# Kernel optimization log

Measured on AMD Instinct MI355X. Metric: run time of the kernel, lower is better.

## Reference

```python
import jax, jax.numpy as jnp
import numpy as np
from jax import lax

B, S, H, T = 64, 512, 1024, 21


def setup_inputs() -> dict:
    key = jax.random.key(0)
    k1, k2, k3, k4, k5, k6, k7 = jax.random.split(key, 7)
    hidden_states = jax.random.normal(k1, (B, S, H), dtype=jnp.float32)
    attention_mask = jnp.ones((B, S), dtype=jnp.int32)
    labels = jax.random.randint(k2, (B, S), 0, T).astype(jnp.int64)
    W = jax.random.normal(k3, (T, H), dtype=jnp.float32) * 0.02
    b = jnp.zeros((T,), dtype=jnp.float32)
    # torchcrf init: uniform(-0.1, 0.1)
    transitions = jax.random.uniform(k4, (T, T), minval=-0.1, maxval=0.1, dtype=jnp.float32)
    start_transitions = jax.random.uniform(k5, (T,), minval=-0.1, maxval=0.1, dtype=jnp.float32)
    end_transitions = jax.random.uniform(k6, (T,), minval=-0.1, maxval=0.1, dtype=jnp.float32)
    return {
        "hidden_states": hidden_states,
        "attention_mask": attention_mask,
        "labels": labels,
        "W": W,
        "b": b,
        "transitions": transitions,
        "start_transitions": start_transitions,
        "end_transitions": end_transitions,
    }


def _crf_log_likelihood(emissions, labels, mask, trans, start, end):
    # emissions [B,S,T], labels [B,S] int, mask [B,S] bool. reduction='sum'.
    Bn, Sn, Tn = emissions.shape
    maskf = mask.astype(emissions.dtype)
    emit_scores = jnp.take_along_axis(emissions, labels[:, :, None], axis=2)[:, :, 0]  # [B,S]
    trans_scores = trans[labels[:, :-1], labels[:, 1:]]  # [B,S-1]
    numerator = start[labels[:, 0]] + emit_scores[:, 0]
    numerator = numerator + jnp.sum((trans_scores + emit_scores[:, 1:]) * maskf[:, 1:], axis=1)
    seq_ends = jnp.sum(mask.astype(jnp.int32), axis=1) - 1  # [B]
    last_tags = labels[jnp.arange(Bn), seq_ends]
    numerator = numerator + end[last_tags]
    # partition via forward algorithm (scan over time)
    alpha0 = start[None, :] + emissions[:, 0]  # [B,T]
    def step(alpha, inp):
        emit_t, mask_t = inp  # [B,T], [B]
        nxt = jax.nn.logsumexp(alpha[:, :, None] + trans[None, :, :] + emit_t[:, None, :], axis=1)
        return jnp.where(mask_t[:, None], nxt, alpha), None
    alpha, _ = lax.scan(step, alpha0, (emissions[:, 1:].transpose(1, 0, 2), mask[:, 1:].T))
    log_Z = jax.nn.logsumexp(alpha + end[None, :], axis=1)  # [B]
    return jnp.sum(numerator - log_Z)


def _viterbi_decode(emissions, mask, trans, start, end):
    Bn, Sn, Tn = emissions.shape
    score0 = start[None, :] + emissions[:, 0]  # [B,T]
    identity_bp = jnp.broadcast_to(jnp.arange(Tn)[None, :], (Bn, Tn))
    def fwd(score, inp):
        emit_t, mask_t = inp
        broad = score[:, :, None] + trans[None, :, :]  # [B, prev, cur]
        best_prev = jnp.argmax(broad, axis=1)  # [B,T]
        nxt = jnp.max(broad, axis=1) + emit_t
        new_score = jnp.where(mask_t[:, None], nxt, score)
        bp = jnp.where(mask_t[:, None], best_prev, identity_bp)
        return new_score, bp
    final_score, bps = lax.scan(fwd, score0, (emissions[:, 1:].transpose(1, 0, 2), mask[:, 1:].T))
    last_tag = jnp.argmax(final_score + end[None, :], axis=1)  # [B] tag at pos S-1
    def back(tag, bp_t):
        prev = jnp.take_along_axis(bp_t, tag[:, None], axis=1)[:, 0]
        return prev, tag
    tag0, tags_rest = lax.scan(back, last_tag, bps, reverse=True)  # tags_rest[t] = tag at pos t+1
    tags = jnp.concatenate([tag0[None, :], tags_rest], axis=0).T  # [B,S]
    return jnp.where(mask, tags, 0).astype(jnp.int64)


def reference(hidden_states, attention_mask, labels, W, b, transitions, start_transitions, end_transitions):
    mask = attention_mask.astype(bool)
    # dropout is identity in eval mode
    emissions = jnp.einsum("bsh,th->bst", hidden_states, W) + b  # [B,S,T]
    log_prob = _crf_log_likelihood(emissions, labels, mask, transitions, start_transitions, end_transitions)
    loss = -log_prob
    pred = _viterbi_decode(emissions, mask, transitions, start_transitions, end_transitions)
    return loss, pred
```

## Files before the change

### kernel.cpp

```cpp
#include <hip/hip_runtime.h>
#include <math.h>
#include <stdint.h>

#define BB 64
#define SS 512
#define HH 1024
#define TT 21

template <int CTRL>
__device__ __forceinline__ float dpp_add(float v) {
  int t = __builtin_amdgcn_update_dpp(0, __float_as_int(v), CTRL, 0xF, 0xF, true);
  return v + __int_as_float(t);
}
__device__ __forceinline__ float wave_sum(float v) {
  v = dpp_add<0x121>(v);
  v = dpp_add<0x122>(v);
  v = dpp_add<0x124>(v);
  v = dpp_add<0x128>(v);
  v += __shfl_xor(v, 16);
  v += __shfl_xor(v, 32);
  return v;
}

#define DOT4(A, H, WV)    \
  A = fmaf(H.x, WV.x, A); \
  A = fmaf(H.y, WV.y, A); \
  A = fmaf(H.z, WV.z, A); \
  A = fmaf(H.w, WV.w, A)

__global__ __launch_bounds__(192, 4) void k_emis(const float* __restrict__ hs,
                                                 const float* __restrict__ W,
                                                 const float* __restrict__ bias,
                                                 float* __restrict__ emis) {
  __shared__ float part[192 * 14];
  const int tid = threadIdx.x;
  const int q = tid & 7;
  const int tmp = tid >> 3;
  const int tg = tmp % 3;
  const int rp = tmp / 3;
  const size_t row0 = (size_t)blockIdx.x * 16 + rp * 2;
  const float4* hp0 = (const float4*)(hs + row0 * HH);
  const float4* hp1 = (const float4*)(hs + (row0 + 1) * HH);
  const float* wb0 = W + (size_t)(tg * 7) * HH + q * 4;

  float a0[7] = {0.f, 0.f, 0.f, 0.f, 0.f, 0.f, 0.f};
  float a1[7] = {0.f, 0.f, 0.f, 0.f, 0.f, 0.f, 0.f};
  float4 h0 = hp0[q], h1 = hp1[q];
#pragma unroll 2
  for (int i = 0; i < 32; ++i) {
    const float4 hc0 = h0, hc1 = h1;
    if (i < 31) {
      h0 = hp0[(i + 1) * 8 + q];
      h1 = hp1[(i + 1) * 8 + q];
    }
    const float* wb = wb0 + (size_t)i * 32;
#pragma unroll
    for (int lt = 0; lt < 7; ++lt) {
      const float4 w = *(const float4*)(wb + (size_t)lt * HH);
      DOT4(a0[lt], hc0, w);
      DOT4(a1[lt], hc1, w);
    }
  }
#pragma unroll
  for (int lt = 0; lt < 7; ++lt) {
    part[tid * 14 + lt] = a0[lt];
    part[tid * 14 + 7 + lt] = a1[lt];
  }
  __syncthreads();

  for (int o = tid; o < 16 * TT; o += 192) {
    const int rr = o / TT;
    const int t = o - rr * TT;
    const int tg2 = t / 7;
    const int lt2 = t - tg2 * 7;
    const float* pp = part + (((rr >> 1) * 3 + tg2) * 8) * 14 + (rr & 1) * 7 + lt2;
    float s = ((pp[0] + pp[14]) + (pp[28] + pp[42])) +
              ((pp[56] + pp[70]) + (pp[84] + pp[98]));
    emis[(size_t)blockIdx.x * (16 * TT) + o] = s + bias[t];
  }
}

#define RLF(V, K) __int_as_float(__builtin_amdgcn_readlane(__float_as_int(V), K))

__global__ __launch_bounds__(64, 1) void k_scan(const float* __restrict__ emis,
                                                const int* __restrict__ mask,
                                                const float* __restrict__ trans,
                                                const float* __restrict__ sv,
                                                const float* __restrict__ ev,
                                                float* __restrict__ logZ,
                                                float* __restrict__ pred) {
  __shared__ unsigned char bp[SS][32];
  __shared__ unsigned char sTag[SS];
  const int lane = threadIdx.x;
  const int j = lane;
  const bool act = (j < TT);
  const int jj = act ? j : 0;
  const int b = blockIdx.x & 63;
  const float* eb = emis + (size_t)b * SS * TT + jj;
  const int4* mq = (const int4*)(mask + b * SS);

  if (blockIdx.x < 64) {
    float E[TT];
#pragma unroll
    for (int i = 0; i < TT; ++i) E[i] = __expf(trans[i * TT + jj]);
    float v = act ? __expf(sv[jj] + eb[0]) : 0.f;
    float C = 0.f;
    float pre[8], cur[8];
#pragma unroll
    for (int k = 0; k < 8; ++k) pre[k] = eb[(size_t)(1 + k) * TT];
    int4 qA = mq[0];
    for (int c = 0; c < 64; ++c) {
      const int base = c * 8;
      const int4 qB = mq[2 * c + 1];
      const int4 qC = mq[(2 * c + 2 < 128) ? (2 * c + 2) : 127];
      float ge[8];
#pragma unroll
      for (int k = 0; k < 8; ++k) cur[k] = pre[k];
#pragma unroll
      for (int k = 0; k < 8; ++k) ge[k] = __expf(cur[k]);
      if (c < 63) {
#pragma unroll
        for (int k = 0; k < 8; ++k) {
          int tl = base + 9 + k;
          tl = (tl < SS) ? tl : (SS - 1);
          pre[k] = eb[(size_t)tl * TT];
        }
      }
      const int mks[8] = {qA.y, qA.z, qA.w, qB.x, qB.y, qB.z, qB.w, qC.x};
#pragma unroll
      for (int p = 0; p < 8; ++p) {
        const int t = base + 1 + p;
        if (t >= SS) break;
        const int mk = mks[p];
        const float ge_t = ge[p];
        const float v0 = RLF(v, 0), v1 = RLF(v, 1), v2 = RLF(v, 2);
        const float v3 = RLF(v, 3), v4 = RLF(v, 4), v5 = RLF(v, 5);
        const float v6 = RLF(v, 6), v7 = RLF(v, 7), v8 = RLF(v, 8);
        const float v9 = RLF(v, 9), v10 = RLF(v, 10), v11 = RLF(v, 11);
        const float v12 = RLF(v, 12), v13 = RLF(v, 13), v14 = RLF(v, 14);
        const float v15 = RLF(v, 15), v16 = RLF(v, 16), v17 = RLF(v, 17);
        const float v18 = RLF(v, 18), v19 = RLF(v, 19), v20 = RLF(v, 20);
        float scale = 1.0f;
        if (p == 7) {
          float m = fmaxf(fmaxf(fmaxf(v0, v1), fmaxf(v2, v3)),
                          fmaxf(fmaxf(v4, v5), fmaxf(v6, v7)));
          m = fmaxf(m, fmaxf(fmaxf(v8, v9), fmaxf(v10, v11)));
          m = fmaxf(m, fmaxf(fmaxf(v12, v13), fmaxf(v14, v15)));
          m = fmaxf(m, fmaxf(fmaxf(v16, v17), fmaxf(v18, v19)));
          m = fmaxf(m, v20);
          int ex = (int)((__float_as_uint(m) >> 23) & 255u) - 127;
          scale = __uint_as_float((unsigned)(127 - ex) << 23);
          C += (float)ex * 0.6931471805599453f;
          v *= scale;
        }
        float q0 = v0 * E[0], q1 = v1 * E[1], q2 = v2 * E[2];
        q0 = fmaf(v3, E[3], q0);   q1 = fmaf(v4, E[4], q1);   q2 = fmaf(v5, E[5], q2);
        q0 = fmaf(v6, E[6], q0);   q1 = fmaf(v7, E[7], q1);   q2 = fmaf(v8, E[8], q2);
        q0 = fmaf(v9, E[9], q0);   q1 = fmaf(v10, E[10], q1); q2 = fmaf(v11, E[11], q2);
        q0 = fmaf(v12, E[12], q0); q1 = fmaf(v13, E[13], q1); q2 = fmaf(v14, E[14], q2);
        q0 = fmaf(v15, E[15], q0); q1 = fmaf(v16, E[16], q1); q2 = fmaf(v17, E[17], q2);
        q0 = fmaf(v18, E[18], q0); q1 = fmaf(v19, E[19], q1); q2 = fmaf(v20, E[20], q2);
        float vn = ((q0 + q1 + q2) * scale) * ge_t;
        v = (act && mk) ? vn : v;
      }
      qA = qC;
    }
    float wv = act ? v * __expf(ev[jj]) : 0.f;
#pragma unroll
    for (int d = 32; d >= 1; d >>= 1) wv += __shfl_xor(wv, d);
    if (lane == 0) logZ[b] = C + __logf(wv);
  } else {
    float Tc[TT];
#pragma unroll
    for (int i = 0; i < TT; ++i) Tc[i] = trans[i * TT + jj];
    float sc = act ? (sv[jj] + eb[0]) : -3.0e38f;
    float pre[8], cur[8];
#pragma unroll
    for (int k = 0; k < 8; ++k) pre[k] = eb[(size_t)(1 + k) * TT];
    int4 qA = mq[0];
    for (int c = 0; c < 64; ++c) {
      const int base = c * 8;
      const int4 qB = mq[2 * c + 1];
      const int4 qC = mq[(2 * c + 2 < 128) ? (2 * c + 2) : 127];
#pragma unroll
      for (int k = 0; k < 8; ++k) cur[k] = pre[k];
      if (c < 63) {
#pragma unroll
        for (int k = 0; k < 8; ++k) {
          int tl = base + 9 + k;
          tl = (tl < SS) ? tl : (SS - 1);
          pre[k] = eb[(size_t)tl * TT];
        }
      }
      const int mks[8] = {qA.y, qA.z, qA.w, qB.x, qB.y, qB.z, qB.w, qC.x};
#pragma unroll
      for (int p = 0; p < 8; ++p) {
        const int t = base + 1 + p;
        if (t >= SS) break;
        const int mk = mks[p];
        const float e = cur[p];
        const float s0 = RLF(sc, 0), s1 = RLF(sc, 1), s2 = RLF(sc, 2);
        const float s3 = RLF(sc, 3), s4 = RLF(sc, 4), s5 = RLF(sc, 5);
        const float s6 = RLF(sc, 6), s7 = RLF(sc, 7), s8 = RLF(sc, 8);
        const float s9 = RLF(sc, 9), s10 = RLF(sc, 10), s11 = RLF(sc, 11);
        const float s12 = RLF(sc, 12), s13 = RLF(sc, 13), s14 = RLF(sc, 14);
        const float s15 = RLF(sc, 15), s16 = RLF(sc, 16), s17 = RLF(sc, 17);
        const float s18 = RLF(sc, 18), s19 = RLF(sc, 19), s20 = RLF(sc, 20);
        float b0v, b1v, b2v;
        int i0, i1, i2;
#define ARGSTEP(BV, BI, VAL, IDX)          \
  {                                        \
    float x_ = (VAL) + Tc[IDX];            \
    if (x_ > BV) { BV = x_; BI = (IDX); }  \
  }
        b0v = s0 + Tc[0]; i0 = 0;
        b1v = s1 + Tc[1]; i1 = 1;
        b2v = s2 + Tc[2]; i2 = 2;
        ARGSTEP(b0v, i0, s3, 3);   ARGSTEP(b1v, i1, s4, 4);   ARGSTEP(b2v, i2, s5, 5);
        ARGSTEP(b0v, i0, s6, 6);   ARGSTEP(b1v, i1, s7, 7);   ARGSTEP(b2v, i2, s8, 8);
        ARGSTEP(b0v, i0, s9, 9);   ARGSTEP(b1v, i1, s10, 10); ARGSTEP(b2v, i2, s11, 11);
        ARGSTEP(b0v, i0, s12, 12); ARGSTEP(b1v, i1, s13, 13); ARGSTEP(b2v, i2, s14, 14);
        ARGSTEP(b0v, i0, s15, 15); ARGSTEP(b1v, i1, s16, 16); ARGSTEP(b2v, i2, s17, 17);
        ARGSTEP(b0v, i0, s18, 18); ARGSTEP(b1v, i1, s19, 19); ARGSTEP(b2v, i2, s20, 20);
#undef ARGSTEP
        float best = b0v;
        int bi = i0;
        if (b1v > best || (b1v == best && i1 < bi)) { best = b1v; bi = i1; }
        if (b2v > best || (b2v == best && i2 < bi)) { best = b2v; bi = i2; }
        float ns = best + e;
        sc = (act && mk) ? ns : sc;
        if (act) bp[t][j] = (unsigned char)(mk ? bi : j);
      }
      qA = qC;
    }
    float fsv = act ? (sc + ev[jj]) : -3.0e38f;
    int idx = j;
#pragma unroll
    for (int d = 32; d >= 1; d >>= 1) {
      float ov = __shfl_xor(fsv, d);
      int oi = __shfl_xor(idx, d);
      bool take = (ov > fsv) || (ov == fsv && oi < idx);
      fsv = take ? ov : fsv;
      idx = take ? oi : idx;
    }
    __syncthreads();
    if (lane == 0) {
      int tag = idx;
      sTag[SS - 1] = (unsigned char)tag;
      for (int t = SS - 1; t >= 1; --t) {
        tag = bp[t][tag];
        sTag[t - 1] = (unsigned char)tag;
      }
    }
    __syncthreads();
    for (int i = lane; i < SS; i += 64) {
      pred[(size_t)b * SS + i] = (float)(mask[b * SS + i] ? (int)sTag[i] : 0);
    }
  }
}

__global__ __launch_bounds__(64, 1) void k_loss(const float* __restrict__ emis,
                                                const int* __restrict__ mask,
                                                const int* __restrict__ labels,
                                                const float* __restrict__ trans,
                                                const float* __restrict__ sv,
                                                const float* __restrict__ ev,
                                                const float* __restrict__ logZ,
                                                float* __restrict__ outv) {
  const int b = blockIdx.x;
  const int lane = threadIdx.x;
  float p = 0.f;
  int cnt = 0;
  for (int t = lane; t < SS; t += 64) {
    cnt += mask[b * SS + t] ? 1 : 0;
    if (t >= 1) {
      const int lp = labels[b * SS + t - 1];
      const int lc = labels[b * SS + t];
      const float mk = (float)mask[b * SS + t];
      p += mk * (trans[lp * TT + lc] + emis[((size_t)b * SS + t) * TT + lc]);
    }
  }
  p = wave_sum(p);
#pragma unroll
  for (int d = 32; d >= 1; d >>= 1) cnt += __shfl_xor(cnt, d);
  if (lane == 0) {
    const int l0 = labels[b * SS];
    float numer = p + sv[l0] + emis[(size_t)b * SS * TT + l0];
    numer += ev[labels[b * SS + cnt - 1]];
    atomicAdd(outv, logZ[b] - numer);
  }
}

extern "C" void kernel_launch(void* const* d_in, const int* in_sizes, int n_in,
                              void* d_out, int out_size, void* d_ws, size_t ws_size,
                              hipStream_t stream) {
  const float* hs = (const float*)d_in[0];
  const int* msk = (const int*)d_in[1];
  const int* lab = (const int*)d_in[2];
  const float* W = (const float*)d_in[3];
  const float* bias = (const float*)d_in[4];
  const float* trans = (const float*)d_in[5];
  const float* sv = (const float*)d_in[6];
  const float* ev = (const float*)d_in[7];
  float* out = (float*)d_out;

  float* emis = (float*)d_ws;
  float* logZ = emis + (size_t)BB * SS * TT;

  hipMemsetAsync(d_out, 0, 4, stream);
  k_emis<<<2048, 192, 0, stream>>>(hs, W, bias, emis);
  k_scan<<<128, 64, 0, stream>>>(emis, msk, trans, sv, ev, logZ, out + 1);
  k_loss<<<64, 64, 0, stream>>>(emis, msk, lab, trans, sv, ev, logZ, out);
}
```

Before: 432.1 us.

## Stage per-sequence emissions in LDS and pack mask into scalar bitmasks

Each scan block first copies its whole sequence's emissions (512x21 floats, about 43KB) into shared memory with vectorized loads, then reads per-step emissions from LDS instead of global memory. The mask is compressed into 64-bit ballot words, and each 64-step window is moved into scalar registers so per-step mask checks become bit extracts. This takes global-load latency off the serial recurrence at the cost of an upfront copy, a barrier and a large LDS allocation.

```diff
diff --git a/kernel.cpp b/kernel.cpp
--- a/kernel.cpp
+++ b/kernel.cpp
@@ -89,6 +89,8 @@
                                                 const float* __restrict__ ev,
                                                 float* __restrict__ logZ,
                                                 float* __restrict__ pred) {
+  __shared__ float sE[SS * TT];
+  __shared__ unsigned long long mb[9];
   __shared__ unsigned char bp[SS][32];
   __shared__ unsigned char sTag[SS];
   const int lane = threadIdx.x;
@@ -96,75 +98,100 @@
   const bool act = (j < TT);
   const int jj = act ? j : 0;
   const int b = blockIdx.x & 63;
-  const float* eb = emis + (size_t)b * SS * TT + jj;
-  const int4* mq = (const int4*)(mask + b * SS);
+
+  {
+    const float4* src = (const float4*)(emis + (size_t)b * SS * TT);
+    float4* dst = (float4*)sE;
+    for (int i = lane; i < SS * TT / 4; i += 64) dst[i] = src[i];
+#pragma unroll
+    for (int w = 0; w < 8; ++w) {
+      unsigned long long bm = __ballot(mask[b * SS + w * 64 + lane] != 0);
+      if (lane == 0) mb[w] = bm;
+    }
+    if (lane == 0) mb[8] = 0ull;
+  }
+  __syncthreads();
 
   if (blockIdx.x < 64) {
     float E[TT];
 #pragma unroll
     for (int i = 0; i < TT; ++i) E[i] = __expf(trans[i * TT + jj]);
-    float v = act ? __expf(sv[jj] + eb[0]) : 0.f;
+    float v = act ? __expf(sv[jj] + sE[jj]) : 0.f;
     float C = 0.f;
-    float pre[8], cur[8];
-#pragma unroll
-    for (int k = 0; k < 8; ++k) pre[k] = eb[(size_t)(1 + k) * TT];
-    int4 qA = mq[0];
-    for (int c = 0; c < 64; ++c) {
-      const int base = c * 8;
-      const int4 qB = mq[2 * c + 1];
-      const int4 qC = mq[(2 * c + 2 < 128) ? (2 * c + 2) : 127];
-      float ge[8];
-#pragma unroll
-      for (int k = 0; k < 8; ++k) cur[k] = pre[k];
-#pragma unroll
-      for (int k = 0; k < 8; ++k) ge[k] = __expf(cur[k]);
-      if (c < 63) {
+    float nxtv[8];
+#pragma unroll
+    for (int k = 0; k < 8; ++k) nxtv[k] = sE[(1 + k) * TT + jj];
+
+#define CRF_STEP(P, SHB)                                                      \
+  {                                                                           \
+    const int mk = (int)((swin >> ((SHB) + (P))) & 1ull);                     \
+    const float ge_t = ge[P];                                                 \
+    const float v0 = RLF(v, 0), v1 = RLF(v, 1), v2 = RLF(v, 2);               \
+    const float v3 = RLF(v, 3), v4 = RLF(v, 4), v5 = RLF(v, 5);               \
+    const float v6 = RLF(v, 6), v7 = RLF(v, 7), v8 = RLF(v, 8);               \
+    const float v9 = RLF(v, 9), v10 = RLF(v, 10), v11 = RLF(v, 11);           \
+    const float v12 = RLF(v, 12), v13 = RLF(v, 13), v14 = RLF(v, 14);         \
+    const float v15 = RLF(v, 15), v16 = RLF(v, 16), v17 = RLF(v, 17);         \
+    const float v18 = RLF(v, 18), v19 = RLF(v, 19), v20 = RLF(v, 20);         \
+    float scale = 1.0f;                                                       \
+    if ((P) == 7) {                                                           \
+      float m = fmaxf(fmaxf(fmaxf(v0, v1), fmaxf(v2, v3)),                    \
+                      fmaxf(fmaxf(v4, v5), fmaxf(v6, v7)));                   \
+      m = fmaxf(m, fmaxf(fmaxf(v8, v9), fmaxf(v10, v11)));                    \
+      m = fmaxf(m, fmaxf(fmaxf(v12, v13), fmaxf(v14, v15)));                  \
+      m = fmaxf(m, fmaxf(fmaxf(v16, v17), fmaxf(v18, v19)));                  \
+      m = fmaxf(m, v20);                                                      \
+      int ex = (int)((__float_as_uint(m) >> 23) & 255u) - 127;                \
+      scale = __uint_as_float((unsigned)(127 - ex) << 23);                    \
+      C += (float)ex * 0.6931471805599453f;                                   \
+      v *= scale;                                                             \
+    }                                                                         \
+    float q0 = v0 * E[0], q1 = v1 * E[1], q2 = v2 * E[2];                     \
+    q0 = fmaf(v3, E[3], q0);   q1 = fmaf(v4, E[4], q1);   q2 = fmaf(v5, E[5], q2);   \
+    q0 = fmaf(v6, E[6], q0);   q1 = fmaf(v7, E[7], q1);   q2 = fmaf(v8, E[8], q2);   \
+    q0 = fmaf(v9, E[9], q0);   q1 = fmaf(v10, E[10], q1); q2 = fmaf(v11, E[11], q2); \
+    q0 = fmaf(v12, E[12], q0); q1 = fmaf(v13, E[13], q1); q2 = fmaf(v14, E[14], q2); \
+    q0 = fmaf(v15, E[15], q0); q1 = fmaf(v16, E[16], q1); q2 = fmaf(v17, E[17], q2); \
+    q0 = fmaf(v18, E[18], q0); q1 = fmaf(v19, E[19], q1); q2 = fmaf(v20, E[20], q2); \
+    float vn = ((q0 + q1 + q2) * scale) * ge_t;                               \
+    v = (act && mk) ? vn : v;                                                 \
+  }
+
+    for (int w = 0; w < 8; ++w) {
+      const unsigned long long wa = mb[w], wb2 = mb[w + 1];
+      const unsigned long long winv = (wa >> 1) | (wb2 << 63);
+      const unsigned wlo = __builtin_amdgcn_readfirstlane((unsigned)winv);
+      const unsigned whi = __builtin_amdgcn_readfirstlane((unsigned)(winv >> 32));
+      const unsigned long long swin = ((unsigned long long)whi << 32) | wlo;
+      const int nci = (w < 7) ? 8 : 7;
+      for (int ci = 0; ci < nci; ++ci) {
+        const int t0 = ((w << 3) + ci) * 8 + 1;
+        float cur[8], ge[8];
+#pragma unroll
+        for (int k = 0; k < 8; ++k) cur[k] = nxtv[k];
+#pragma unroll
+        for (int k = 0; k < 8; ++k) ge[k] = __expf(cur[k]);
 #pragma unroll
         for (int k = 0; k < 8; ++k) {
-          int tl = base + 9 + k;
+          int tl = t0 + 8 + k;
           tl = (tl < SS) ? tl : (SS - 1);
-          pre[k] = eb[(size_t)tl * TT];
+          nxtv[k] = sE[tl * TT + jj];
         }
-      }
-      const int mks[8] = {qA.y, qA.z, qA.w, qB.x, qB.y, qB.z, qB.w, qC.x};
-#pragma unroll
-      for (int p = 0; p < 8; ++p) {
-        const int t = base + 1 + p;
-        if (t >= SS) break;
-        const int mk = mks[p];
-        const float ge_t = ge[p];
-        const float v0 = RLF(v, 0), v1 = RLF(v, 1), v2 = RLF(v, 2);
-        const float v3 = RLF(v, 3), v4 = RLF(v, 4), v5 = RLF(v, 5);
-        const float v6 = RLF(v, 6), v7 = RLF(v, 7), v8 = RLF(v, 8);
-        const float v9 = RLF(v, 9), v10 = RLF(v, 10), v11 = RLF(v, 11);
-        const float v12 = RLF(v, 12), v13 = RLF(v, 13), v14 = RLF(v, 14);
-        const float v15 = RLF(v, 15), v16 = RLF(v, 16), v17 = RLF(v, 17);
-        const float v18 = RLF(v, 18), v19 = RLF(v, 19), v20 = RLF(v, 20);
-        float scale = 1.0f;
-        if (p == 7) {
-          float m = fmaxf(fmaxf(fmaxf(v0, v1), fmaxf(v2, v3)),
-                          fmaxf(fmaxf(v4, v5), fmaxf(v6, v7)));
-          m = fmaxf(m, fmaxf(fmaxf(v8, v9), fmaxf(v10, v11)));
-          m = fmaxf(m, fmaxf(fmaxf(v12, v13), fmaxf(v14, v15)));
-          m = fmaxf(m, fmaxf(fmaxf(v16, v17), fmaxf(v18, v19)));
-          m = fmaxf(m, v20);
-          int ex = (int)((__float_as_uint(m) >> 23) & 255u) - 127;
-          scale = __uint_as_float((unsigned)(127 - ex) << 23);
-          C += (float)ex * 0.6931471805599453f;
-          v *= scale;
-        }
-        float q0 = v0 * E[0], q1 = v1 * E[1], q2 = v2 * E[2];
-        q0 = fmaf(v3, E[3], q0);   q1 = fmaf(v4, E[4], q1);   q2 = fmaf(v5, E[5], q2);
-        q0 = fmaf(v6, E[6], q0);   q1 = fmaf(v7, E[7], q1);   q2 = fmaf(v8, E[8], q2);
-        q0 = fmaf(v9, E[9], q0);   q1 = fmaf(v10, E[10], q1); q2 = fmaf(v11, E[11], q2);
-        q0 = fmaf(v12, E[12], q0); q1 = fmaf(v13, E[13], q1); q2 = fmaf(v14, E[14], q2);
-        q0 = fmaf(v15, E[15], q0); q1 = fmaf(v16, E[16], q1); q2 = fmaf(v17, E[17], q2);
-        q0 = fmaf(v18, E[18], q0); q1 = fmaf(v19, E[19], q1); q2 = fmaf(v20, E[20], q2);
-        float vn = ((q0 + q1 + q2) * scale) * ge_t;
-        v = (act && mk) ? vn : v;
-      }
-      qA = qC;
-    }
+        const int shb = ci << 3;
+#pragma unroll
+        for (int p = 0; p < 8; ++p) { CRF_STEP(p, shb); }
+      }
+      if (w == 7) {
+        float cur[8], ge[8];
+#pragma unroll
+        for (int k = 0; k < 7; ++k) cur[k] = nxtv[k];
+#pragma unroll
+        for (int k = 0; k < 7; ++k) ge[k] = __expf(cur[k]);
+#pragma unroll
+        for (int p = 0; p < 7; ++p) { CRF_STEP(p, 56); }
+      }
+    }
+#undef CRF_STEP
     float wv = act ? v * __expf(ev[jj]) : 0.f;
 #pragma unroll
     for (int d = 32; d >= 1; d >>= 1) wv += __shfl_xor(wv, d);
@@ -173,66 +200,79 @@
     float Tc[TT];
 #pragma unroll
     for (int i = 0; i < TT; ++i) Tc[i] = trans[i * TT + jj];
-    float sc = act ? (sv[jj] + eb[0]) : -3.0e38f;
-    float pre[8], cur[8];
-#pragma unroll
-    for (int k = 0; k < 8; ++k) pre[k] = eb[(size_t)(1 + k) * TT];
-    int4 qA = mq[0];
-    for (int c = 0; c < 64; ++c) {
-      const int base = c * 8;
-      const int4 qB = mq[2 * c + 1];
-      const int4 qC = mq[(2 * c + 2 < 128) ? (2 * c + 2) : 127];
-#pragma unroll
-      for (int k = 0; k < 8; ++k) cur[k] = pre[k];
-      if (c < 63) {
-#pragma unroll
-        for (int k = 0; k < 8; ++k) {
-          int tl = base + 9 + k;
-          tl = (tl < SS) ? tl : (SS - 1);
-          pre[k] = eb[(size_t)tl * TT];
-        }
-      }
-      const int mks[8] = {qA.y, qA.z, qA.w, qB.x, qB.y, qB.z, qB.w, qC.x};
-#pragma unroll
-      for (int p = 0; p < 8; ++p) {
-        const int t = base + 1 + p;
-        if (t >= SS) break;
-        const int mk = mks[p];
-        const float e = cur[p];
-        const float s0 = RLF(sc, 0), s1 = RLF(sc, 1), s2 = RLF(sc, 2);
-        const float s3 = RLF(sc, 3), s4 = RLF(sc, 4), s5 = RLF(sc, 5);
-        const float s6 = RLF(sc, 6), s7 = RLF(sc, 7), s8 = RLF(sc, 8);
-        const float s9 = RLF(sc, 9), s10 = RLF(sc, 10), s11 = RLF(sc, 11);
-        const float s12 = RLF(sc, 12), s13 = RLF(sc, 13), s14 = RLF(sc, 14);
-        const float s15 = RLF(sc, 15), s16 = RLF(sc, 16), s17 = RLF(sc, 17);
-        const float s18 = RLF(sc, 18), s19 = RLF(sc, 19), s20 = RLF(sc, 20);
-        float b0v, b1v, b2v;
-        int i0, i1, i2;
+    float sc = act ? (sv[jj] + sE[jj]) : -3.0e38f;
+    float nxtv[8];
+#pragma unroll
+    for (int k = 0; k < 8; ++k) nxtv[k] = sE[(1 + k) * TT + jj];
+
 #define ARGSTEP(BV, BI, VAL, IDX)          \
   {                                        \
     float x_ = (VAL) + Tc[IDX];            \
     if (x_ > BV) { BV = x_; BI = (IDX); }  \
   }
-        b0v = s0 + Tc[0]; i0 = 0;
-        b1v = s1 + Tc[1]; i1 = 1;
-        b2v = s2 + Tc[2]; i2 = 2;
-        ARGSTEP(b0v, i0, s3, 3);   ARGSTEP(b1v, i1, s4, 4);   ARGSTEP(b2v, i2, s5, 5);
-        ARGSTEP(b0v, i0, s6, 6);   ARGSTEP(b1v, i1, s7, 7);   ARGSTEP(b2v, i2, s8, 8);
-        ARGSTEP(b0v, i0, s9, 9);   ARGSTEP(b1v, i1, s10, 10); ARGSTEP(b2v, i2, s11, 11);
-        ARGSTEP(b0v, i0, s12, 12); ARGSTEP(b1v, i1, s13, 13); ARGSTEP(b2v, i2, s14, 14);
-        ARGSTEP(b0v, i0, s15, 15); ARGSTEP(b1v, i1, s16, 16); ARGSTEP(b2v, i2, s17, 17);
-        ARGSTEP(b0v, i0, s18, 18); ARGSTEP(b1v, i1, s19, 19); ARGSTEP(b2v, i2, s20, 20);
+#define VIT_STEP(P, SHB, TCUR)                                                \
+  {                                                                           \
+    const int mk = (int)((swin >> ((SHB) + (P))) & 1ull);                     \
+    const float e = cur[P];                                                   \
+    const float s0 = RLF(sc, 0), s1 = RLF(sc, 1), s2 = RLF(sc, 2);            \
+    const float s3 = RLF(sc, 3), s4 = RLF(sc, 4), s5 = RLF(sc, 5);            \
+    const float s6 = RLF(sc, 6), s7 = RLF(sc, 7), s8 = RLF(sc, 8);            \
+    const float s9 = RLF(sc, 9), s10 = RLF(sc, 10), s11 = RLF(sc, 11);        \
+    const float s12 = RLF(sc, 12), s13 = RLF(sc, 13), s14 = RLF(sc, 14);      \
+    const float s15 = RLF(sc, 15), s16 = RLF(sc, 16), s17 = RLF(sc, 17);      \
+    const float s18 = RLF(sc, 18), s19 = RLF(sc, 19), s20 = RLF(sc, 20);      \
+    float b0v, b1v, b2v;                                                      \
+    int i0, i1, i2;                                                           \
+    b0v = s0 + Tc[0]; i0 = 0;                                                 \
+    b1v = s1 + Tc[1]; i1 = 1;                                                 \
+    b2v = s2 + Tc[2]; i2 = 2;                                                 \
+    ARGSTEP(b0v, i0, s3, 3);   ARGSTEP(b1v, i1, s4, 4);   ARGSTEP(b2v, i2, s5, 5);    \
+    ARGSTEP(b0v, i0, s6, 6);   ARGSTEP(b1v, i1, s7, 7);   ARGSTEP(b2v, i2, s8, 8);    \
+    ARGSTEP(b0v, i0, s9, 9);   ARGSTEP(b1v, i1, s10, 10); ARGSTEP(b2v, i2, s11, 11);  \
+    ARGSTEP(b0v, i0, s12, 12); ARGSTEP(b1v, i1, s13, 13); ARGSTEP(b2v, i2, s14, 14);  \
+    ARGSTEP(b0v, i0, s15, 15); ARGSTEP(b1v, i1, s16, 16); ARGSTEP(b2v, i2, s17, 17);  \
+    ARGSTEP(b0v, i0, s18, 18); ARGSTEP(b1v, i1, s19, 19); ARGSTEP(b2v, i2, s20, 20);  \
+    float best = b0v;                                                         \
+    int bi = i0;                                                              \
+    if (b1v > best || (b1v == best && i1 < bi)) { best = b1v; bi = i1; }      \
+    if (b2v > best || (b2v == best && i2 < bi)) { best = b2v; bi = i2; }      \
+    float ns = best + e;                                                      \
+    sc = (act && mk) ? ns : sc;                                               \
+    if (act) bp[TCUR][j] = (unsigned char)(mk ? bi : j);                      \
+  }
+
+    for (int w = 0; w < 8; ++w) {
+      const unsigned long long wa = mb[w], wb2 = mb[w + 1];
+      const unsigned long long winv = (wa >> 1) | (wb2 << 63);
+      const unsigned wlo = __builtin_amdgcn_readfirstlane((unsigned)winv);
+      const unsigned whi = __builtin_amdgcn_readfirstlane((unsigned)(winv >> 32));
+      const unsigned long long swin = ((unsigned long long)whi << 32) | wlo;
+      const int nci = (w < 7) ? 8 : 7;
+      for (int ci = 0; ci < nci; ++ci) {
+        const int t0 = ((w << 3) + ci) * 8 + 1;
+        float cur[8];
+#pragma unroll
+        for (int k = 0; k < 8; ++k) cur[k] = nxtv[k];
+#pragma unroll
+        for (int k = 0; k < 8; ++k) {
+          int tl = t0 + 8 + k;
+          tl = (tl < SS) ? tl : (SS - 1);
+          nxtv[k] = sE[tl * TT + jj];
+        }
+        const int shb = ci << 3;
+#pragma unroll
+        for (int p = 0; p < 8; ++p) { VIT_STEP(p, shb, t0 + p); }
+      }
+      if (w == 7) {
+        float cur[8];
+#pragma unroll
+        for (int k = 0; k < 7; ++k) cur[k] = nxtv[k];
+#pragma unroll
+        for (int p = 0; p < 7; ++p) { VIT_STEP(p, 56, 505 + p); }
+      }
+    }
+#undef VIT_STEP
 #undef ARGSTEP
-        float best = b0v;
-        int bi = i0;
-        if (b1v > best || (b1v == best && i1 < bi)) { best = b1v; bi = i1; }
-        if (b2v > best || (b2v == best && i2 < bi)) { best = b2v; bi = i2; }
-        float ns = best + e;
-        sc = (act && mk) ? ns : sc;
-        if (act) bp[t][j] = (unsigned char)(mk ? bi : j);
-      }
-      qA = qC;
-    }
     float fsv = act ? (sc + ev[jj]) : -3.0e38f;
     int idx = j;
 #pragma unroll
```

After: 448.9 us. 1.04x slower.
